# Performance work log

Hardware: AMD Instinct MI355X
Metric: run time of the kernel (lower is better)

## Reference

```python
import jax, jax.numpy as jnp
import numpy as np

HEADS = 4
DIM_HEAD = 32


def setup_inputs() -> dict:
    key = jax.random.key(0)
    k1, k2, k3, k4 = jax.random.split(key, 4)
    dim = 256
    hidden = HEADS * DIM_HEAD  # 128
    x = jax.random.normal(k1, (4, dim, 64, 64), dtype=jnp.float32)
    # 1x1 convs are channel-mixing matmuls; store weights as [out_ch, in_ch]
    w_qkv = jax.random.normal(k2, (3 * hidden, dim), dtype=jnp.float32) * (dim ** -0.5)
    w_out = jax.random.normal(k3, (dim, hidden), dtype=jnp.float32) * (hidden ** -0.5)
    b_out = jax.random.normal(k4, (dim,), dtype=jnp.float32) * 0.02
    return {"x": x, "w_qkv": w_qkv, "w_out": w_out, "b_out": b_out}


def reference(x, w_qkv, w_out, b_out):
    b, c, h, w = x.shape
    n = h * w
    scale = DIM_HEAD ** -0.5
    xf = x.reshape(b, c, n)                                   # b c n
    qkv = jnp.einsum('oc,bcn->bon', w_qkv, xf)                # b (3*H*D) n
    q, k, v = jnp.split(qkv, 3, axis=1)                       # each b (H*D) n
    q = q.reshape(b, HEADS, DIM_HEAD, n) * scale              # b h d n
    k = k.reshape(b, HEADS, DIM_HEAD, n)
    v = v.reshape(b, HEADS, DIM_HEAD, n)
    sim = jnp.einsum('bhdi,bhdj->bhij', q, k)                 # b h n n
    attn = jax.nn.softmax(sim, axis=-1)                       # stable max-subtract inside
    out = jnp.einsum('bhij,bhdj->bhdi', attn, v)              # b h d n
    out = out.reshape(b, HEADS * DIM_HEAD, n)                 # b (h d) n
    out = jnp.einsum('oc,bcn->bon', w_out, out) + b_out[None, :, None]
    return out.reshape(b, -1, h, w)
```

## Files before the change

### kernel.cpp

```cpp
#include <hip/hip_runtime.h>
#include <hip/hip_bf16.h>
#include <stdint.h>

#define B_SZ 4
#define C_IN 256
#define N_SP 4096
#define HEADS 4
#define DH 32
#define HID 128

#define BI 128
#define BJ 64
#define PP 68

typedef short short4v __attribute__((ext_vector_type(4)));
typedef short short8 __attribute__((ext_vector_type(8)));
typedef float f32x4 __attribute__((ext_vector_type(4)));

#if __has_builtin(__builtin_amdgcn_exp2f)
#define EXP2 __builtin_amdgcn_exp2f
#else
#define EXP2 exp2f
#endif

__device__ __forceinline__ short f2bfs(float f) {
  return (short)((__float_as_uint(f) + 0x8000u) >> 16);
}
__device__ __forceinline__ float bfs2f(short s) {
  return __uint_as_float(((uint32_t)(unsigned short)s) << 16);
}
__device__ __forceinline__ uint32_t pk_bf(float a, float b) {
  uint32_t ua = __float_as_uint(a) + 0x8000u;
  uint32_t ub = __float_as_uint(b) + 0x8000u;
  return (ua >> 16) | (ub & 0xffff0000u);
}
__device__ __forceinline__ short8 ld_frag(const short* p) {
  short4v a = *(const short4v*)p;
  short4v b = *(const short4v*)(p + 4);
  return __builtin_shufflevector(a, b, 0, 1, 2, 3, 4, 5, 6, 7);
}
__device__ __forceinline__ f32x4 mfma16(short8 a, short8 b, f32x4 c) {
  return __builtin_amdgcn_mfma_f32_16x16x32_bf16(a, b, c, 0, 0, 0);
}

__global__ __launch_bounds__(256) void prep_k(
    const float* __restrict__ x, const float* __restrict__ w_qkv,
    const float* __restrict__ w_out,
    short* __restrict__ xh, short* __restrict__ xl,
    short* __restrict__ wqh, short* __restrict__ wql,
    short* __restrict__ woh, short* __restrict__ wol) {
  const int t = threadIdx.x;
  const int bx = blockIdx.x;
  if (bx < 256) {
    __shared__ float T[64 * 65];
    const int b = bx >> 6, n0 = (bx & 63) * 64;
    const float* xb = x + (size_t)b * C_IN * N_SP;
    for (int c0 = 0; c0 < C_IN; c0 += 64) {
      {
        const int n = t & 63, cw = t >> 6;
#pragma unroll
        for (int i = 0; i < 16; ++i) {
          const int c = cw * 16 + i;
          T[n * 65 + c] = xb[(size_t)(c0 + c) * N_SP + n0 + n];
        }
      }
      __syncthreads();
      {
        const int n = t >> 2, cg = t & 3;
#pragma unroll
        for (int j = 0; j < 2; ++j) {
          const int c = cg * 16 + j * 8;
          short8 hv, lv;
#pragma unroll
          for (int e = 0; e < 8; ++e) {
            const float v = T[n * 65 + c + e];
            const short hh = f2bfs(v);
            hv[e] = hh;
            lv[e] = f2bfs(v - bfs2f(hh));
          }
          const size_t off = ((size_t)(b * N_SP + n0 + n)) * C_IN + c0 + c;
          *(short8*)(xh + off) = hv;
          *(short8*)(xl + off) = lv;
        }
      }
      __syncthreads();
    }
  } else {
    const int f0 = (bx - 256) * 8192;
#pragma unroll
    for (int j = 0; j < 32; ++j) {
      const int f = f0 + j * 256 + t;
      float v;
      short *dh, *dl;
      int idx;
      if (f < 384 * 256) { v = w_qkv[f]; dh = wqh; dl = wql; idx = f; }
      else { idx = f - 384 * 256; v = w_out[idx]; dh = woh; dl = wol; }
      const short hh = f2bfs(v);
      dh[idx] = hh;
      dl[idx] = f2bfs(v - bfs2f(hh));
    }
  }
}

__global__ __launch_bounds__(256) void qkv_mfma_k(
    const short* __restrict__ xh, const short* __restrict__ xl,
    const short* __restrict__ wqh, const short* __restrict__ wql,
    short* __restrict__ qt, short* __restrict__ kt, short* __restrict__ vt) {
  const int t = threadIdx.x;
  const int lane = t & 63, w = t >> 6;
  const int l15 = lane & 15, quad = lane >> 4;
  const int osec = blockIdx.y, b = blockIdx.z;
  const int n0 = blockIdx.x * 64 + w * 16;
  const size_t xrow = ((size_t)(b * N_SP + n0 + l15)) * C_IN;
  const size_t wrow = ((size_t)(osec * 128 + l15)) * C_IN;
  const bool isv = (osec == 2);
  const f32x4 zz = {0.f, 0.f, 0.f, 0.f};
  f32x4 acc[8];
#pragma unroll
  for (int ot = 0; ot < 8; ++ot) acc[ot] = zz;

  for (int k0 = 0; k0 < C_IN; k0 += 32) {
    const int ko = k0 + quad * 8;
    const short8 xhf = *(const short8*)(xh + xrow + ko);
    const short8 xlf = *(const short8*)(xl + xrow + ko);
#pragma unroll
    for (int ot = 0; ot < 8; ++ot) {
      const size_t wo = wrow + (size_t)ot * 16 * C_IN + ko;
      const short8 whf = *(const short8*)(wqh + wo);
      const short8 wlf = *(const short8*)(wql + wo);
      if (isv) {
        acc[ot] = mfma16(xhf, whf, acc[ot]);
        acc[ot] = mfma16(xlf, whf, acc[ot]);
        acc[ot] = mfma16(xhf, wlf, acc[ot]);
      } else {
        acc[ot] = mfma16(whf, xhf, acc[ot]);
        acc[ot] = mfma16(whf, xlf, acc[ot]);
        acc[ot] = mfma16(wlf, xhf, acc[ot]);
      }
    }
  }

  if (!isv) {
    const float sc = osec ? 1.f : (0.17677669529663687f * 1.4426950408889634f);
    short* dst = osec ? kt : qt;
    const int n = n0 + l15;
#pragma unroll
    for (int ot = 0; ot < 8; ++ot) {
      const int ol = ot * 16 + quad * 4;
      const int h = ol >> 5, d0 = ol & 31;
      short4v p;
#pragma unroll
      for (int r = 0; r < 4; ++r) p[r] = f2bfs(acc[ot][r] * sc);
      *(short4v*)(dst + ((size_t)(b * HEADS + h) * N_SP + n) * DH + d0) = p;
    }
  } else {
    const int n = n0 + quad * 4;
#pragma unroll
    for (int ot = 0; ot < 8; ++ot) {
      const int ol = ot * 16 + l15;
      const int h = ol >> 5, d = ol & 31;
      short4v p;
#pragma unroll
      for (int r = 0; r < 4; ++r) p[r] = f2bfs(acc[ot][r]);
      *(short4v*)(vt + ((size_t)(b * HEADS + h) * DH + d) * N_SP + n) = p;
    }
  }
}

__global__ __launch_bounds__(256, 2) void attn_k(
    const short* __restrict__ qt, const short* __restrict__ kt,
    const short* __restrict__ vt, short* __restrict__ ath,
    short* __restrict__ atl) {
  __shared__ short Ps[BI * PP];
  __shared__ float Osh[DH * 132];
  const int t = threadIdx.x;
  const int lane = t & 63, w = t >> 6;
  const int l15 = lane & 15, quad = lane >> 4;
  const int i0 = blockIdx.x * BI;
  const int bh = blockIdx.y;
  const short* qg = qt + ((size_t)bh * N_SP + i0) * DH;
  const short* kg = kt + (size_t)bh * N_SP * DH;
  const short* vg = vt + (size_t)bh * DH * N_SP;

  short8 bq[2];
#pragma unroll
  for (int tt = 0; tt < 2; ++tt)
    bq[tt] = *(const short8*)(qg + (size_t)(w * 32 + tt * 16 + l15) * DH + quad * 8);

  const f32x4 zz = {0.f, 0.f, 0.f, 0.f};
  f32x4 o_acc[2][2] = {{zz, zz}, {zz, zz}};
  float lsum[2] = {0.f, 0.f};
  short* prow[2];
#pragma unroll
  for (int tt = 0; tt < 2; ++tt) prow[tt] = Ps + (w * 32 + tt * 16 + l15) * PP;

  short8 akA[4], akB[4], vbA[2][2], vbB[2][2];
#pragma unroll
  for (int jt = 0; jt < 4; ++jt)
    akA[jt] = *(const short8*)(kg + (size_t)(jt * 16 + l15) * DH + quad * 8);
#pragma unroll
  for (int dt = 0; dt < 2; ++dt)
#pragma unroll
    for (int kk = 0; kk < 2; ++kk)
      vbA[dt][kk] = *(const short8*)(vg + (size_t)(dt * 16 + l15) * N_SP + kk * 32 + quad * 8);

  auto body = [&](const short8 (&akc)[4], const short8 (&vbc)[2][2],
                  short8 (&akn)[4], short8 (&vbn)[2][2], int jn) {
    f32x4 sf[2][4];
#pragma unroll
    for (int tt = 0; tt < 2; ++tt)
#pragma unroll
      for (int jt = 0; jt < 4; ++jt) sf[tt][jt] = mfma16(akc[jt], bq[tt], zz);
#pragma unroll
    for (int jt = 0; jt < 4; ++jt)
      akn[jt] = *(const short8*)(kg + (size_t)(jn + jt * 16 + l15) * DH + quad * 8);
#pragma unroll
    for (int dt = 0; dt < 2; ++dt)
#pragma unroll
      for (int kk = 0; kk < 2; ++kk)
        vbn[dt][kk] = *(const short8*)(vg + (size_t)(dt * 16 + l15) * N_SP + jn + kk * 32 + quad * 8);
#pragma unroll
    for (int tt = 0; tt < 2; ++tt)
#pragma unroll
      for (int jt = 0; jt < 4; ++jt) {
        const float e0 = EXP2(sf[tt][jt][0]);
        const float e1 = EXP2(sf[tt][jt][1]);
        const float e2 = EXP2(sf[tt][jt][2]);
        const float e3 = EXP2(sf[tt][jt][3]);
        lsum[tt] += (e0 + e1) + (e2 + e3);
        uint2 pk; pk.x = pk_bf(e0, e1); pk.y = pk_bf(e2, e3);
        *(uint2*)(prow[tt] + jt * 16 + quad * 4) = pk;
      }
    asm volatile("s_waitcnt lgkmcnt(0)" ::: "memory");
    short8 pa[2][2];
#pragma unroll
    for (int tt = 0; tt < 2; ++tt)
#pragma unroll
      for (int kk = 0; kk < 2; ++kk) pa[tt][kk] = ld_frag(prow[tt] + kk * 32 + quad * 8);
#pragma unroll
    for (int tt = 0; tt < 2; ++tt)
#pragma unroll
      for (int dt = 0; dt < 2; ++dt) {
        o_acc[tt][dt] = mfma16(pa[tt][0], vbc[dt][0], o_acc[tt][dt]);
        o_acc[tt][dt] = mfma16(pa[tt][1], vbc[dt][1], o_acc[tt][dt]);
      }
  };

  for (int jt0 = 0; jt0 < N_SP; jt0 += 2 * BJ) {
    body(akA, vbA, akB, vbB, (jt0 + BJ) & (N_SP - 1));
    body(akB, vbB, akA, vbA, (jt0 + 2 * BJ) & (N_SP - 1));
  }

#pragma unroll
  for (int tt = 0; tt < 2; ++tt) {
    lsum[tt] += __shfl_xor(lsum[tt], 16);
    lsum[tt] += __shfl_xor(lsum[tt], 32);
  }
  float linv[2][4];
#pragma unroll
  for (int tt = 0; tt < 2; ++tt)
#pragma unroll
    for (int r = 0; r < 4; ++r) linv[tt][r] = 1.f / __shfl(lsum[tt], quad * 4 + r);
#pragma unroll
  for (int tt = 0; tt < 2; ++tt)
#pragma unroll
    for (int dt = 0; dt < 2; ++dt)
#pragma unroll
      for (int r = 0; r < 4; ++r)
        Osh[(dt * 16 + l15) * 132 + w * 32 + tt * 16 + quad * 4 + r] =
            o_acc[tt][dt][r] * linv[tt][r];
  __syncthreads();
  {
    const int ii = t & 127, half = t >> 7;
    const int b = bh >> 2, h = bh & 3;
#pragma unroll
    for (int j = 0; j < 2; ++j) {
      short8 hv, lv;
#pragma unroll
      for (int e = 0; e < 8; ++e) {
        const int d = half * 16 + j * 8 + e;
        const float v = Osh[d * 132 + ii];
        const short hh = f2bfs(v);
        hv[e] = hh;
        lv[e] = f2bfs(v - bfs2f(hh));
      }
      const size_t off =
          ((size_t)(b * N_SP + i0 + ii)) * HID + h * 32 + half * 16 + j * 8;
      *(short8*)(ath + off) = hv;
      *(short8*)(atl + off) = lv;
    }
  }
}

__global__ __launch_bounds__(256) void out_mfma_k(
    const short* __restrict__ ath, const short* __restrict__ atl,
    const short* __restrict__ woh, const short* __restrict__ wol,
    const float* __restrict__ bias, float* __restrict__ out) {
  const int t = threadIdx.x;
  const int lane = t & 63, w = t >> 6;
  const int l15 = lane & 15, quad = lane >> 4;
  const int osec = blockIdx.y, b = blockIdx.z;
  const int n0 = blockIdx.x * 64 + w * 16;
  const size_t arow = ((size_t)(b * N_SP + n0 + l15)) * HID;
  const size_t wrow = ((size_t)(osec * 128 + l15)) * HID;
  const f32x4 zz = {0.f, 0.f, 0.f, 0.f};
  f32x4 acc[8];
#pragma unroll
  for (int ot = 0; ot < 8; ++ot) acc[ot] = zz;

  for (int k0 = 0; k0 < HID; k0 += 32) {
    const int ko = k0 + quad * 8;
    const short8 ahf = *(const short8*)(ath + arow + ko);
    const short8 alf = *(const short8*)(atl + arow + ko);
#pragma unroll
    for (int ot = 0; ot < 8; ++ot) {
      const size_t wo = wrow + (size_t)ot * 16 * HID + ko;
      const short8 whf = *(const short8*)(woh + wo);
      const short8 wlf = *(const short8*)(wol + wo);
      acc[ot] = mfma16(ahf, whf, acc[ot]);
      acc[ot] = mfma16(alf, whf, acc[ot]);
      acc[ot] = mfma16(ahf, wlf, acc[ot]);
    }
  }
#pragma unroll
  for (int ot = 0; ot < 8; ++ot) {
    const int o = osec * 128 + ot * 16 + l15;
    const float bv = bias[o];
    float4 v = make_float4(acc[ot][0] + bv, acc[ot][1] + bv,
                           acc[ot][2] + bv, acc[ot][3] + bv);
    *(float4*)(out + ((size_t)(b * C_IN + o)) * N_SP + n0 + quad * 4) = v;
  }
}

extern "C" void kernel_launch(void* const* d_in, const int* in_sizes, int n_in,
                              void* d_out, int out_size, void* d_ws, size_t ws_size,
                              hipStream_t stream) {
  const float* x = (const float*)d_in[0];
  const float* w_qkv = (const float*)d_in[1];
  const float* w_out = (const float*)d_in[2];
  const float* b_out = (const float*)d_in[3];
  float* out = (float*)d_out;

  short* xh = (short*)d_ws;
  short* xl = xh + (size_t)B_SZ * N_SP * C_IN;
  short* wqh = xl + (size_t)B_SZ * N_SP * C_IN;
  short* wql = wqh + 384 * C_IN;
  short* woh = wql + 384 * C_IN;
  short* wol = woh + C_IN * HID;
  short* qt = wol + C_IN * HID;
  short* kt = qt + (size_t)16 * N_SP * DH;
  short* vt = kt + (size_t)16 * N_SP * DH;
  short* ath = xh;
  short* atl = ath + (size_t)B_SZ * N_SP * HID;

  prep_k<<<dim3(272), 256, 0, stream>>>(x, w_qkv, w_out, xh, xl, wqh, wql, woh, wol);
  qkv_mfma_k<<<dim3(64, 3, B_SZ), 256, 0, stream>>>(xh, xl, wqh, wql, qt, kt, vt);
  attn_k<<<dim3(N_SP / BI, B_SZ * HEADS), 256, 0, stream>>>(qt, kt, vt, ath, atl);
  out_mfma_k<<<dim3(64, 2, B_SZ), 256, 0, stream>>>(ath, atl, woh, wol, b_out, out);
}
```

Baseline: 245.6 us.

## Split attention keys into two halves and merge partials in output projection

The attention kernel now splits the key dimension into two halves across a third grid axis. It writes unnormalized fp32 partial outputs and row sums, and the output projection kernel sums and normalizes them before the hi/lo bf16 split. This doubles the number of attention blocks to improve occupancy and CU fill, and raises the occupancy hint to 4. It also adds setprio around the MFMA groups, uses the hardware packed bf16 convert, and splits the prep kernel into more blocks. In exchange the partials travel through global memory as fp32, and the final normalization moves into the output GEMM. The split skips max subtraction, as before, which relies on bounded logits.

```diff
diff --git a/kernel.cpp b/kernel.cpp
--- a/kernel.cpp
+++ b/kernel.cpp
@@ -11,6 +11,7 @@
 
 #define BI 128
 #define BJ 64
+#define JHALF 2048
 #define PP 68
 
 typedef short short4v __attribute__((ext_vector_type(4)));
@@ -28,11 +29,6 @@
 }
 __device__ __forceinline__ float bfs2f(short s) {
   return __uint_as_float(((uint32_t)(unsigned short)s) << 16);
-}
-__device__ __forceinline__ uint32_t pk_bf(float a, float b) {
-  uint32_t ua = __float_as_uint(a) + 0x8000u;
-  uint32_t ub = __float_as_uint(b) + 0x8000u;
-  return (ua >> 16) | (ub & 0xffff0000u);
 }
 __device__ __forceinline__ short8 ld_frag(const short* p) {
   short4v a = *(const short4v*)p;
@@ -51,42 +47,39 @@
     short* __restrict__ woh, short* __restrict__ wol) {
   const int t = threadIdx.x;
   const int bx = blockIdx.x;
-  if (bx < 256) {
+  if (bx < 1024) {
     __shared__ float T[64 * 65];
-    const int b = bx >> 6, n0 = (bx & 63) * 64;
+    const int b = bx >> 8, n0 = ((bx >> 2) & 63) * 64, c0 = (bx & 3) * 64;
     const float* xb = x + (size_t)b * C_IN * N_SP;
-    for (int c0 = 0; c0 < C_IN; c0 += 64) {
-      {
-        const int n = t & 63, cw = t >> 6;
-#pragma unroll
-        for (int i = 0; i < 16; ++i) {
-          const int c = cw * 16 + i;
-          T[n * 65 + c] = xb[(size_t)(c0 + c) * N_SP + n0 + n];
+    {
+      const int n = t & 63, cw = t >> 6;
+#pragma unroll
+      for (int i = 0; i < 16; ++i) {
+        const int c = cw * 16 + i;
+        T[n * 65 + c] = xb[(size_t)(c0 + c) * N_SP + n0 + n];
+      }
+    }
+    __syncthreads();
+    {
+      const int n = t >> 2, cg = t & 3;
+#pragma unroll
+      for (int j = 0; j < 2; ++j) {
+        const int c = cg * 16 + j * 8;
+        short8 hv, lv;
+#pragma unroll
+        for (int e = 0; e < 8; ++e) {
+          const float v = T[n * 65 + c + e];
+          const short hh = f2bfs(v);
+          hv[e] = hh;
+          lv[e] = f2bfs(v - bfs2f(hh));
         }
-      }
-      __syncthreads();
-      {
-        const int n = t >> 2, cg = t & 3;
-#pragma unroll
-        for (int j = 0; j < 2; ++j) {
-          const int c = cg * 16 + j * 8;
-          short8 hv, lv;
-#pragma unroll
-          for (int e = 0; e < 8; ++e) {
-            const float v = T[n * 65 + c + e];
-            const short hh = f2bfs(v);
-            hv[e] = hh;
-            lv[e] = f2bfs(v - bfs2f(hh));
-          }
-          const size_t off = ((size_t)(b * N_SP + n0 + n)) * C_IN + c0 + c;
-          *(short8*)(xh + off) = hv;
-          *(short8*)(xl + off) = lv;
-        }
-      }
-      __syncthreads();
+        const size_t off = ((size_t)(b * N_SP + n0 + n)) * C_IN + c0 + c;
+        *(short8*)(xh + off) = hv;
+        *(short8*)(xl + off) = lv;
+      }
     }
   } else {
-    const int f0 = (bx - 256) * 8192;
+    const int f0 = (bx - 1024) * 8192;
 #pragma unroll
     for (int j = 0; j < 32; ++j) {
       const int f = f0 + j * 256 + t;
@@ -167,10 +160,10 @@
   }
 }
 
-__global__ __launch_bounds__(256, 2) void attn_k(
+__global__ __launch_bounds__(256, 4) void attn_k(
     const short* __restrict__ qt, const short* __restrict__ kt,
-    const short* __restrict__ vt, short* __restrict__ ath,
-    short* __restrict__ atl) {
+    const short* __restrict__ vt, float* __restrict__ po,
+    float* __restrict__ lws) {
   __shared__ short Ps[BI * PP];
   __shared__ float Osh[DH * 132];
   const int t = threadIdx.x;
@@ -178,9 +171,11 @@
   const int l15 = lane & 15, quad = lane >> 4;
   const int i0 = blockIdx.x * BI;
   const int bh = blockIdx.y;
+  const int part = blockIdx.z;
+  const int jbase = part * JHALF;
   const short* qg = qt + ((size_t)bh * N_SP + i0) * DH;
-  const short* kg = kt + (size_t)bh * N_SP * DH;
-  const short* vg = vt + (size_t)bh * DH * N_SP;
+  const short* kg = kt + ((size_t)bh * N_SP + jbase) * DH;
+  const short* vg = vt + (size_t)bh * DH * N_SP + jbase;
 
   short8 bq[2];
 #pragma unroll
@@ -207,10 +202,12 @@
   auto body = [&](const short8 (&akc)[4], const short8 (&vbc)[2][2],
                   short8 (&akn)[4], short8 (&vbn)[2][2], int jn) {
     f32x4 sf[2][4];
+    __builtin_amdgcn_s_setprio(1);
 #pragma unroll
     for (int tt = 0; tt < 2; ++tt)
 #pragma unroll
       for (int jt = 0; jt < 4; ++jt) sf[tt][jt] = mfma16(akc[jt], bq[tt], zz);
+    __builtin_amdgcn_s_setprio(0);
 #pragma unroll
     for (int jt = 0; jt < 4; ++jt)
       akn[jt] = *(const short8*)(kg + (size_t)(jn + jt * 16 + l15) * DH + quad * 8);
@@ -228,7 +225,9 @@
         const float e2 = EXP2(sf[tt][jt][2]);
         const float e3 = EXP2(sf[tt][jt][3]);
         lsum[tt] += (e0 + e1) + (e2 + e3);
-        uint2 pk; pk.x = pk_bf(e0, e1); pk.y = pk_bf(e2, e3);
+        uint2 pk;
+        asm("v_cvt_pk_bf16_f32 %0, %1, %2" : "=v"(pk.x) : "v"(e0), "v"(e1));
+        asm("v_cvt_pk_bf16_f32 %0, %1, %2" : "=v"(pk.y) : "v"(e2), "v"(e3));
         *(uint2*)(prow[tt] + jt * 16 + quad * 4) = pk;
       }
     asm volatile("s_waitcnt lgkmcnt(0)" ::: "memory");
@@ -237,6 +236,7 @@
     for (int tt = 0; tt < 2; ++tt)
 #pragma unroll
       for (int kk = 0; kk < 2; ++kk) pa[tt][kk] = ld_frag(prow[tt] + kk * 32 + quad * 8);
+    __builtin_amdgcn_s_setprio(1);
 #pragma unroll
     for (int tt = 0; tt < 2; ++tt)
 #pragma unroll
@@ -244,11 +244,12 @@
         o_acc[tt][dt] = mfma16(pa[tt][0], vbc[dt][0], o_acc[tt][dt]);
         o_acc[tt][dt] = mfma16(pa[tt][1], vbc[dt][1], o_acc[tt][dt]);
       }
+    __builtin_amdgcn_s_setprio(0);
   };
 
-  for (int jt0 = 0; jt0 < N_SP; jt0 += 2 * BJ) {
-    body(akA, vbA, akB, vbB, (jt0 + BJ) & (N_SP - 1));
-    body(akB, vbB, akA, vbA, (jt0 + 2 * BJ) & (N_SP - 1));
+  for (int jo = 0; jo < JHALF; jo += 2 * BJ) {
+    body(akA, vbA, akB, vbB, (jo + BJ) & (JHALF - 1));
+    body(akB, vbB, akA, vbA, (jo + 2 * BJ) & (JHALF - 1));
   }
 
 #pragma unroll
@@ -256,44 +257,38 @@
     lsum[tt] += __shfl_xor(lsum[tt], 16);
     lsum[tt] += __shfl_xor(lsum[tt], 32);
   }
-  float linv[2][4];
+  if (lane < 16) {
+#pragma unroll
+    for (int tt = 0; tt < 2; ++tt)
+      lws[((size_t)(part * 16 + bh)) * N_SP + i0 + w * 32 + tt * 16 + lane] = lsum[tt];
+  }
 #pragma unroll
   for (int tt = 0; tt < 2; ++tt)
 #pragma unroll
-    for (int r = 0; r < 4; ++r) linv[tt][r] = 1.f / __shfl(lsum[tt], quad * 4 + r);
-#pragma unroll
-  for (int tt = 0; tt < 2; ++tt)
-#pragma unroll
     for (int dt = 0; dt < 2; ++dt)
 #pragma unroll
       for (int r = 0; r < 4; ++r)
-        Osh[(dt * 16 + l15) * 132 + w * 32 + tt * 16 + quad * 4 + r] =
-            o_acc[tt][dt][r] * linv[tt][r];
+        Osh[(dt * 16 + l15) * 132 + w * 32 + tt * 16 + quad * 4 + r] = o_acc[tt][dt][r];
   __syncthreads();
   {
     const int ii = t & 127, half = t >> 7;
     const int b = bh >> 2, h = bh & 3;
-#pragma unroll
-    for (int j = 0; j < 2; ++j) {
-      short8 hv, lv;
-#pragma unroll
-      for (int e = 0; e < 8; ++e) {
-        const int d = half * 16 + j * 8 + e;
-        const float v = Osh[d * 132 + ii];
-        const short hh = f2bfs(v);
-        hv[e] = hh;
-        lv[e] = f2bfs(v - bfs2f(hh));
-      }
-      const size_t off =
-          ((size_t)(b * N_SP + i0 + ii)) * HID + h * 32 + half * 16 + j * 8;
-      *(short8*)(ath + off) = hv;
-      *(short8*)(atl + off) = lv;
+    float* dst = po + ((size_t)((part * B_SZ + b) * N_SP) + i0 + ii) * HID +
+                 h * 32 + half * 16;
+#pragma unroll
+    for (int j4 = 0; j4 < 4; ++j4) {
+      float4 vv;
+      vv.x = Osh[(half * 16 + j4 * 4 + 0) * 132 + ii];
+      vv.y = Osh[(half * 16 + j4 * 4 + 1) * 132 + ii];
+      vv.z = Osh[(half * 16 + j4 * 4 + 2) * 132 + ii];
+      vv.w = Osh[(half * 16 + j4 * 4 + 3) * 132 + ii];
+      *(float4*)(dst + j4 * 4) = vv;
     }
   }
 }
 
 __global__ __launch_bounds__(256) void out_mfma_k(
-    const short* __restrict__ ath, const short* __restrict__ atl,
+    const float* __restrict__ po, const float* __restrict__ lws,
     const short* __restrict__ woh, const short* __restrict__ wol,
     const float* __restrict__ bias, float* __restrict__ out) {
   const int t = threadIdx.x;
@@ -301,7 +296,9 @@
   const int l15 = lane & 15, quad = lane >> 4;
   const int osec = blockIdx.y, b = blockIdx.z;
   const int n0 = blockIdx.x * 64 + w * 16;
-  const size_t arow = ((size_t)(b * N_SP + n0 + l15)) * HID;
+  const int n = n0 + l15;
+  const size_t PSTR = (size_t)B_SZ * N_SP * HID;
+  const float* arow = po + ((size_t)(b * N_SP) + n) * HID;
   const size_t wrow = ((size_t)(osec * 128 + l15)) * HID;
   const f32x4 zz = {0.f, 0.f, 0.f, 0.f};
   f32x4 acc[8];
@@ -310,8 +307,26 @@
 
   for (int k0 = 0; k0 < HID; k0 += 32) {
     const int ko = k0 + quad * 8;
-    const short8 ahf = *(const short8*)(ath + arow + ko);
-    const short8 alf = *(const short8*)(atl + arow + ko);
+    const int h = k0 >> 5;
+    const int bh = b * HEADS + h;
+    const float lv = lws[(size_t)bh * N_SP + n] + lws[(size_t)(16 + bh) * N_SP + n];
+    const float linv = 1.f / lv;
+    const float* pr = arow + ko;
+    const float4 u0 = *(const float4*)(pr);
+    const float4 u1 = *(const float4*)(pr + 4);
+    const float4 v0 = *(const float4*)(pr + PSTR);
+    const float4 v1 = *(const float4*)(pr + PSTR + 4);
+    const float av[8] = {(u0.x + v0.x) * linv, (u0.y + v0.y) * linv,
+                         (u0.z + v0.z) * linv, (u0.w + v0.w) * linv,
+                         (u1.x + v1.x) * linv, (u1.y + v1.y) * linv,
+                         (u1.z + v1.z) * linv, (u1.w + v1.w) * linv};
+    short8 ahf, alf;
+#pragma unroll
+    for (int e = 0; e < 8; ++e) {
+      const short hh = f2bfs(av[e]);
+      ahf[e] = hh;
+      alf[e] = f2bfs(av[e] - bfs2f(hh));
+    }
 #pragma unroll
     for (int ot = 0; ot < 8; ++ot) {
       const size_t wo = wrow + (size_t)ot * 16 * HID + ko;
@@ -350,11 +365,11 @@
   short* qt = wol + C_IN * HID;
   short* kt = qt + (size_t)16 * N_SP * DH;
   short* vt = kt + (size_t)16 * N_SP * DH;
-  short* ath = xh;
-  short* atl = ath + (size_t)B_SZ * N_SP * HID;
-
-  prep_k<<<dim3(272), 256, 0, stream>>>(x, w_qkv, w_out, xh, xl, wqh, wql, woh, wol);
+  float* lws = (float*)(vt + (size_t)16 * N_SP * DH);
+  float* po = (float*)xh;
+
+  prep_k<<<dim3(1040), 256, 0, stream>>>(x, w_qkv, w_out, xh, xl, wqh, wql, woh, wol);
   qkv_mfma_k<<<dim3(64, 3, B_SZ), 256, 0, stream>>>(xh, xl, wqh, wql, qt, kt, vt);
-  attn_k<<<dim3(N_SP / BI, B_SZ * HEADS), 256, 0, stream>>>(qt, kt, vt, ath, atl);
-  out_mfma_k<<<dim3(64, 2, B_SZ), 256, 0, stream>>>(ath, atl, woh, wol, b_out, out);
-}
+  attn_k<<<dim3(N_SP / BI, B_SZ * HEADS, 2), 256, 0, stream>>>(qt, kt, vt, po, lws);
+  out_mfma_k<<<dim3(64, 2, B_SZ), 256, 0, stream>>>(po, lws, woh, wol, b_out, out);
+}
```

New measurement: 286.4 us. +16.6%, slower.
